# Performance work log

Hardware: AMD Instinct MI355X
Metric: run time of the kernel (lower is better)

Reference implementation:

```python
import jax, jax.numpy as jnp
import numpy as np

DIM = 1024          # n_embd
NUM_EXPERTS = 8
TOP_K = 2
HIDDEN = 4 * DIM // TOP_K   # expert_hidden_dim = 2048
BS, SLEN = 1, 2048


def setup_inputs() -> dict:
    key = jax.random.key(0)
    k0, k1, k2, k3 = jax.random.split(key, 4)
    x = jax.random.normal(k0, (BS, SLEN, DIM), dtype=jnp.float32)
    gate_w = jax.random.normal(k1, (NUM_EXPERTS, DIM), dtype=jnp.float32) * 0.02
    w_up = jax.random.normal(k2, (NUM_EXPERTS, HIDDEN, DIM), dtype=jnp.float32) * 0.02
    w_down = jax.random.normal(k3, (NUM_EXPERTS, DIM, HIDDEN), dtype=jnp.float32) * 0.02
    expert_bias = jnp.zeros((NUM_EXPERTS,), dtype=jnp.float32)
    return {"x": x, "gate_w": gate_w, "w_up": w_up, "w_down": w_down,
            "expert_bias": expert_bias}


def _moe(x, gate_w, w_up, w_down, expert_bias):
    bs, slen, dim = x.shape
    xf = x.reshape(-1, dim)                       # (T, D)
    # Sigmoid router (scores in fp32, bias only affects selection, not weights)
    scores = jax.nn.sigmoid(xf @ gate_w.T)        # (T, E)
    biased = scores + expert_bias
    _, sel = jax.lax.top_k(biased, TOP_K)         # (T, K) expert ids, distinct per token
    top_scores = jnp.take_along_axis(scores, sel, axis=-1)  # (T, K)

    # Scatter/gather dispatch + grouped GEMM is mathematically equivalent to:
    #   out[t] = sum_k W_down[e_tk] @ relu(W_up[e_tk] @ (s_tk * x[t]))^2
    # Loop over the small fixed expert set via lax.scan; unassigned tokens
    # contribute exactly zero (relu(0)^2 = 0), honoring the routing sparsity.
    def body(acc, ew):
        e, wu, wd = ew
        # combined routing weight for this expert per token (at most one slot)
        w_t = jnp.sum(jnp.where(sel == e, top_scores, 0.0), axis=-1)  # (T,)
        xe = xf * w_t[:, None]                    # (T, D), zero for non-routed
        h = jnp.square(jax.nn.relu(xe @ wu.T))    # (T, H)  relu(x)^2 activation
        return acc + h @ wd.T, None

    out0 = jnp.zeros_like(xf)
    out, _ = jax.lax.scan(body, out0, (jnp.arange(NUM_EXPERTS), w_up, w_down))
    return out.reshape(bs, slen, dim)


def reference(x, gate_w, w_up, w_down, expert_bias):
    return _moe(x, gate_w, w_up, w_down, expert_bias)
```

## Files before the change

kernel.cpp:

```cpp
#include <hip/hip_runtime.h>
#include <cstdint>
#include <cstddef>

#define T_TOK 2048
#define DMODEL 1024
#define NEXP 8
#define HID 2048
#define DUMP_ID 4096
#define NB_CONV 8192

typedef __bf16 bf16x8 __attribute__((ext_vector_type(8)));
typedef float f32x4 __attribute__((ext_vector_type(4)));
typedef unsigned short u16;
typedef u16 u16x8 __attribute__((ext_vector_type(8)));

__device__ __forceinline__ u16 f2bf(float f) {
    union { float f; unsigned int u; } v; v.f = f;
    unsigned int u = v.u;
    unsigned int r = (u + 0x7FFFu + ((u >> 16) & 1u)) >> 16;
    return (u16)r;
}

__device__ __forceinline__ void gl2lds16(const void* g, void* l) {
    __builtin_amdgcn_global_load_lds(
        (const __attribute__((address_space(1))) void*)g,
        (__attribute__((address_space(3))) void*)l,
        16, 0, 0);
}

__global__ __launch_bounds__(256) void fused_pre(
    const float4* __restrict__ wu4, const float4* __restrict__ wd4,
    ushort4* __restrict__ wub4, ushort4* __restrict__ wdb4,
    const float4* __restrict__ x4, const float4* __restrict__ gw4,
    const float* __restrict__ bias, ushort4* __restrict__ xb4,
    unsigned int* __restrict__ selpack, float* __restrict__ w2,
    unsigned int* __restrict__ xb_dump_row_u32) {
    const int b = blockIdx.x;
    const int tid = threadIdx.x;

    if (b < NB_CONV) {
        const int n4u = NEXP * HID * DMODEL / 4;
        int i0 = b * 256 + tid;
#pragma unroll
        for (int c = 0; c < 4; ++c) {
            int idx = i0 + c * (NB_CONV * 256);
            float4 f = (idx < n4u) ? wu4[idx] : wd4[idx - n4u];
            ushort4 o;
            o.x = f2bf(f.x); o.y = f2bf(f.y); o.z = f2bf(f.z); o.w = f2bf(f.w);
            if (idx < n4u) wub4[idx] = o; else wdb4[idx - n4u] = o;
        }
        return;
    }
    if (b == NB_CONV + 256) {
        if (tid < DMODEL / 2) xb_dump_row_u32[tid] = 0;
        return;
    }
    const int rb = b - NB_CONV;
    const int wv = tid >> 6;
    const int lane = tid & 63;
    const int pair = rb * 4 + wv;
    const int t0 = 2 * pair, t1 = t0 + 1;

    float acc0[NEXP], acc1[NEXP];
#pragma unroll
    for (int e = 0; e < NEXP; ++e) { acc0[e] = 0.f; acc1[e] = 0.f; }
#pragma unroll
    for (int j = 0; j < 4; ++j) {
        int i4 = lane + j * 64;
        float4 a0 = x4[t0 * 256 + i4];
        float4 a1 = x4[t1 * 256 + i4];
        ushort4 s0, s1;
        s0.x = f2bf(a0.x); s0.y = f2bf(a0.y); s0.z = f2bf(a0.z); s0.w = f2bf(a0.w);
        s1.x = f2bf(a1.x); s1.y = f2bf(a1.y); s1.z = f2bf(a1.z); s1.w = f2bf(a1.w);
        xb4[t0 * 256 + i4] = s0;
        xb4[t1 * 256 + i4] = s1;
#pragma unroll
        for (int e = 0; e < NEXP; ++e) {
            float4 g = gw4[e * 256 + i4];
            acc0[e] += a0.x * g.x + a0.y * g.y + a0.z * g.z + a0.w * g.w;
            acc1[e] += a1.x * g.x + a1.y * g.y + a1.z * g.z + a1.w * g.w;
        }
    }
#pragma unroll
    for (int e = 0; e < NEXP; ++e)
        for (int off = 32; off > 0; off >>= 1) {
            acc0[e] += __shfl_xor(acc0[e], off, 64);
            acc1[e] += __shfl_xor(acc1[e], off, 64);
        }
    if (lane == 0) {
#pragma unroll
        for (int tt = 0; tt < 2; ++tt) {
            int t = tt ? t1 : t0;
            float sc[NEXP], bi[NEXP];
#pragma unroll
            for (int e = 0; e < NEXP; ++e) {
                float a = tt ? acc1[e] : acc0[e];
                sc[e] = 1.f / (1.f + expf(-a));
                bi[e] = sc[e] + bias[e];
            }
            int e0 = 0;
            for (int e = 1; e < NEXP; ++e) if (bi[e] > bi[e0]) e0 = e;
            int e1 = -1;
            for (int e = 0; e < NEXP; ++e) {
                if (e == e0) continue;
                if (e1 < 0 || bi[e] > bi[e1]) e1 = e;
            }
            selpack[t] = (unsigned int)e0 | ((unsigned int)e1 << 8);
            w2[2 * t]     = sc[e0] * sc[e0];
            w2[2 * t + 1] = sc[e1] * sc[e1];
        }
    }
}

__global__ __launch_bounds__(256) void build_lists(
    const unsigned int* __restrict__ selpack, int* __restrict__ counts,
    int* __restrict__ list) {
    const int e = blockIdx.x;
    const int tid = threadIdx.x;
    const int lane = tid & 63;
    const int wv = tid >> 6;
    __shared__ int wsum[4];
    __shared__ int base;
    if (tid == 0) base = 0;
    __syncthreads();
    for (int tb = 0; tb < T_TOK; tb += 256) {
        int t = tb + tid;
        unsigned int sp = selpack[t];
        bool f1 = ((sp >> 8) & 255u) == (unsigned)e;
        bool f = ((sp & 255u) == (unsigned)e) | f1;
        int id = 2 * t + (f1 ? 1 : 0);
        unsigned long long m = __ballot(f);
        int pos = __popcll(m & ((1ull << lane) - 1ull));
        if (lane == 0) wsum[wv] = __popcll(m);
        __syncthreads();
        int woff = 0;
#pragma unroll
        for (int i = 0; i < 4; ++i) if (i < wv) woff += wsum[i];
        int bse = base;
        if (f) list[e * T_TOK + bse + woff + pos] = id;
        __syncthreads();
        if (tid == 0) base = bse + wsum[0] + wsum[1] + wsum[2] + wsum[3];
    }
    __syncthreads();
    int total = base;
    if (tid == 0) counts[e] = total;
    for (int i = total + tid; i < T_TOK; i += 256) list[e * T_TOK + i] = DUMP_ID;
}

template <int MODE>
__global__ __launch_bounds__(256, 2) void moe_gemm(
    const u16* __restrict__ Asrc, const int* __restrict__ list,
    const int* __restrict__ counts, const u16* __restrict__ Ball,
    const float* __restrict__ w2, u16* __restrict__ Hout,
    float* __restrict__ Cout) {
    constexpr int K   = (MODE == 0) ? DMODEL : HID;
    constexpr int N   = (MODE == 0) ? HID : DMODEL;
    constexpr int NKT = K / 64;
    constexpr int NTN = N / 128;
    constexpr int LOGNTN = (MODE == 0) ? 4 : 3;

    const int b = blockIdx.x;
    const int e = b & 7;
    const int rest = b >> 3;
    const int m0 = (rest >> LOGNTN) * 128;
    if (m0 >= counts[e]) return;
    const int n0 = (rest & (NTN - 1)) * 128;

    const int tid = threadIdx.x;
    const int lane = tid & 63;
    const int w = tid >> 6;

    __shared__ u16 As[128 * 64];
    __shared__ u16 Bs[128 * 64];

    const int* mylist = list + e * T_TOK + m0;
    const u16* B = Ball + (size_t)e * HID * DMODEL;

    const u16* ap[4];
    const u16* bp[4];
#pragma unroll
    for (int it = 0; it < 4; ++it) {
        int row = it * 32 + (tid >> 3);
        int gs = (tid & 7) ^ (row & 7);
        int id = mylist[row];
        int arow = (MODE == 0) ? (id >> 1) : id;
        ap[it] = Asrc + (size_t)arow * K + gs * 8;
        bp[it] = B + (size_t)(n0 + row) * K + gs * 8;
    }

    const int wm = (w >> 1) * 64;
    const int wn = (w & 1) * 64;
    const int quad = lane >> 4;
    const int lrow = lane & 15;

    f32x4 acc[4][4];
#pragma unroll
    for (int i = 0; i < 4; ++i)
#pragma unroll
        for (int j = 0; j < 4; ++j) acc[i][j] = f32x4{0.f, 0.f, 0.f, 0.f};

    for (int kt = 0; kt < NKT; ++kt) {
#pragma unroll
        for (int it = 0; it < 4; ++it)
            gl2lds16(ap[it] + kt * 64, &As[(it * 256 + w * 64) * 8]);
#pragma unroll
        for (int it = 0; it < 4; ++it)
            gl2lds16(bp[it] + kt * 64, &Bs[(it * 256 + w * 64) * 8]);
        __syncthreads();
#pragma unroll
        for (int s = 0; s < 2; ++s) {
            const int q = s * 4 + quad;
            bf16x8 af[4], bfr[4];
#pragma unroll
            for (int i = 0; i < 4; ++i) {
                int ra = wm + i * 16 + lrow;
                int rb = wn + i * 16 + lrow;
                af[i]  = *(const bf16x8*)&As[ra * 64 + (q ^ (ra & 7)) * 8];
                bfr[i] = *(const bf16x8*)&Bs[rb * 64 + (q ^ (rb & 7)) * 8];
            }
#pragma unroll
            for (int i = 0; i < 4; ++i)
#pragma unroll
                for (int j = 0; j < 4; ++j)
                    acc[i][j] = __builtin_amdgcn_mfma_f32_16x16x32_bf16(
                        af[i], bfr[j], acc[i][j], 0, 0, 0);
        }
        __syncthreads();
    }

#pragma unroll
    for (int i = 0; i < 4; ++i) {
        int mbase = wm + i * 16 + (lane >> 4) * 4;
        int ids[4];
        float ww[4];
#pragma unroll
        for (int r = 0; r < 4; ++r) {
            ids[r] = mylist[mbase + r];
            if (MODE == 0) ww[r] = w2[ids[r]];
        }
#pragma unroll
        for (int j = 0; j < 4; ++j) {
            int n = n0 + wn + j * 16 + (lane & 15);
#pragma unroll
            for (int r = 0; r < 4; ++r) {
                float v = acc[i][j][r];
                if (MODE == 0) {
                    v = (v > 0.f) ? v * v * ww[r] : 0.f;
                    Hout[(size_t)ids[r] * HID + n] = f2bf(v);
                } else {
                    if (ids[r] != DUMP_ID)
                        atomicAdd(&Cout[(size_t)(ids[r] >> 1) * DMODEL + n], v);
                }
            }
        }
    }
}

extern "C" void kernel_launch(void* const* d_in, const int* in_sizes, int n_in,
                              void* d_out, int out_size, void* d_ws, size_t ws_size,
                              hipStream_t stream) {
    const float* x      = (const float*)d_in[0];
    const float* gate_w = (const float*)d_in[1];
    const float* w_up   = (const float*)d_in[2];
    const float* w_down = (const float*)d_in[3];
    const float* bias   = (const float*)d_in[4];
    float* out = (float*)d_out;

    char* p = (char*)d_ws;
    int* counts = (int*)p;                 p += 256;
    int* list   = (int*)p;                 p += NEXP * T_TOK * 4;
    float* w2   = (float*)p;               p += 4104 * 4;
    unsigned int* selpack = (unsigned int*)p;  p += T_TOK * 4;
    u16* xb  = (u16*)p;  p += (size_t)(T_TOK + 1) * DMODEL * 2;
    u16* wub = (u16*)p;  p += (size_t)NEXP * HID * DMODEL * 2;
    u16* wdb = (u16*)p;  p += (size_t)NEXP * HID * DMODEL * 2;
    u16* h   = (u16*)p;  p += (size_t)(2 * T_TOK + 1) * HID * 2;

    hipMemsetAsync(d_out, 0, (size_t)out_size * sizeof(float), stream);

    fused_pre<<<NB_CONV + 256 + 1, 256, 0, stream>>>(
        (const float4*)w_up, (const float4*)w_down,
        (ushort4*)wub, (ushort4*)wdb,
        (const float4*)x, (const float4*)gate_w, bias,
        (ushort4*)xb, selpack, w2,
        (unsigned int*)(xb + (size_t)T_TOK * DMODEL));

    build_lists<<<NEXP, 256, 0, stream>>>(selpack, counts, list);

    moe_gemm<0><<<16 * (HID / 128) * NEXP, 256, 0, stream>>>(
        xb, list, counts, wub, w2, h, nullptr);

    moe_gemm<1><<<16 * (DMODEL / 128) * NEXP, 256, 0, stream>>>(
        h, list, counts, wdb, w2, nullptr, out);
}
```

Measured before the change: 265.6 us.

## Overlap w_down bf16 conversion with the up-projection GEMM launch

The fp32-to-bf16 conversion of w_down moves out of the pre-processing kernel and into extra blocks appended to the first grouped GEMM. Those blocks can then overlap with the up-projection GEMM tiles, shortening the critical path of the pre-kernel. The trade-off is that conversion blocks compete with GEMM blocks for CUs and bandwidth, and block scheduling order decides how much overlap actually happens.

```diff
diff --git a/kernel.cpp b/kernel.cpp
--- a/kernel.cpp
+++ b/kernel.cpp
@@ -7,7 +7,7 @@
 #define NEXP 8
 #define HID 2048
 #define DUMP_ID 4096
-#define NB_CONV 8192
+#define NB_CONV 4096
 
 typedef __bf16 bf16x8 __attribute__((ext_vector_type(8)));
 typedef float f32x4 __attribute__((ext_vector_type(4)));
@@ -28,9 +28,22 @@
         16, 0, 0);
 }
 
+__device__ __forceinline__ void cvt_blk(const float4* __restrict__ src,
+                                        ushort4* __restrict__ dst,
+                                        int bc, int tid) {
+    const int S = NB_CONV * 256;
+    const int i0 = bc * 256 + tid;
+#pragma unroll
+    for (int c = 0; c < 4; ++c) {
+        float4 f = src[i0 + c * S];
+        ushort4 o;
+        o.x = f2bf(f.x); o.y = f2bf(f.y); o.z = f2bf(f.z); o.w = f2bf(f.w);
+        dst[i0 + c * S] = o;
+    }
+}
+
 __global__ __launch_bounds__(256) void fused_pre(
-    const float4* __restrict__ wu4, const float4* __restrict__ wd4,
-    ushort4* __restrict__ wub4, ushort4* __restrict__ wdb4,
+    const float4* __restrict__ wu4, ushort4* __restrict__ wub4,
     const float4* __restrict__ x4, const float4* __restrict__ gw4,
     const float* __restrict__ bias, ushort4* __restrict__ xb4,
     unsigned int* __restrict__ selpack, float* __restrict__ w2,
@@ -39,16 +52,7 @@
     const int tid = threadIdx.x;
 
     if (b < NB_CONV) {
-        const int n4u = NEXP * HID * DMODEL / 4;
-        int i0 = b * 256 + tid;
-#pragma unroll
-        for (int c = 0; c < 4; ++c) {
-            int idx = i0 + c * (NB_CONV * 256);
-            float4 f = (idx < n4u) ? wu4[idx] : wd4[idx - n4u];
-            ushort4 o;
-            o.x = f2bf(f.x); o.y = f2bf(f.y); o.z = f2bf(f.z); o.w = f2bf(f.w);
-            if (idx < n4u) wub4[idx] = o; else wdb4[idx - n4u] = o;
-        }
+        cvt_blk(wu4, wub4, b, tid);
         return;
     }
     if (b == NB_CONV + 256) {
@@ -152,21 +156,29 @@
     const u16* __restrict__ Asrc, const int* __restrict__ list,
     const int* __restrict__ counts, const u16* __restrict__ Ball,
     const float* __restrict__ w2, u16* __restrict__ Hout,
-    float* __restrict__ Cout) {
+    float* __restrict__ Cout,
+    const float4* __restrict__ cvt_src, ushort4* __restrict__ cvt_dst) {
     constexpr int K   = (MODE == 0) ? DMODEL : HID;
     constexpr int N   = (MODE == 0) ? HID : DMODEL;
     constexpr int NKT = K / 64;
     constexpr int NTN = N / 128;
     constexpr int LOGNTN = (MODE == 0) ? 4 : 3;
+    constexpr int GEMMB = (T_TOK / 128) * NTN * NEXP;
 
     const int b = blockIdx.x;
+    const int tid = threadIdx.x;
+
+    if (MODE == 0 && b >= GEMMB) {
+        cvt_blk(cvt_src, cvt_dst, b - GEMMB, tid);
+        return;
+    }
+
     const int e = b & 7;
     const int rest = b >> 3;
     const int m0 = (rest >> LOGNTN) * 128;
     if (m0 >= counts[e]) return;
     const int n0 = (rest & (NTN - 1)) * 128;
 
-    const int tid = threadIdx.x;
     const int lane = tid & 63;
     const int w = tid >> 6;
 
@@ -279,17 +291,18 @@
     hipMemsetAsync(d_out, 0, (size_t)out_size * sizeof(float), stream);
 
     fused_pre<<<NB_CONV + 256 + 1, 256, 0, stream>>>(
-        (const float4*)w_up, (const float4*)w_down,
-        (ushort4*)wub, (ushort4*)wdb,
+        (const float4*)w_up, (ushort4*)wub,
         (const float4*)x, (const float4*)gate_w, bias,
         (ushort4*)xb, selpack, w2,
         (unsigned int*)(xb + (size_t)T_TOK * DMODEL));
 
     build_lists<<<NEXP, 256, 0, stream>>>(selpack, counts, list);
 
-    moe_gemm<0><<<16 * (HID / 128) * NEXP, 256, 0, stream>>>(
-        xb, list, counts, wub, w2, h, nullptr);
+    moe_gemm<0><<<16 * (HID / 128) * NEXP + NB_CONV, 256, 0, stream>>>(
+        xb, list, counts, wub, w2, h, nullptr,
+        (const float4*)w_down, (ushort4*)wdb);
 
     moe_gemm<1><<<16 * (DMODEL / 128) * NEXP, 256, 0, stream>>>(
-        h, list, counts, wdb, w2, nullptr, out);
-}
+        h, list, counts, wdb, w2, nullptr, out,
+        nullptr, nullptr);
+}
```

Measured after the change: 274.3 us. 1.03x slower.

## Fuse fp32-to-bf16 weight conversion into grouped GEMM B-tile loads

Applied to the files above, without the earlier changes.

Removes the separate pre-pass that converted all expert up/down weights from fp32 to bf16 in a workspace. The GEMM kernels now read fp32 weights directly through registers, convert them to bf16 and write swizzled tiles into LDS, replacing the async global-to-LDS copy for B. This avoids writing and re-reading 64 MB of bf16 weights, but each weight tile is now read as fp32 (twice the bytes) by every M-tile that uses it. It also loses the direct-to-LDS load path and adds conversion ALU work inside the K loop.

```diff
diff --git a/kernel.cpp b/kernel.cpp
--- a/kernel.cpp
+++ b/kernel.cpp
@@ -7,7 +7,6 @@
 #define NEXP 8
 #define HID 2048
 #define DUMP_ID 4096
-#define NB_CONV 8192
 
 typedef __bf16 bf16x8 __attribute__((ext_vector_type(8)));
 typedef float f32x4 __attribute__((ext_vector_type(4)));
@@ -29,8 +28,6 @@
 }
 
 __global__ __launch_bounds__(256) void fused_pre(
-    const float4* __restrict__ wu4, const float4* __restrict__ wd4,
-    ushort4* __restrict__ wub4, ushort4* __restrict__ wdb4,
     const float4* __restrict__ x4, const float4* __restrict__ gw4,
     const float* __restrict__ bias, ushort4* __restrict__ xb4,
     unsigned int* __restrict__ selpack, float* __restrict__ w2,
@@ -38,27 +35,13 @@
     const int b = blockIdx.x;
     const int tid = threadIdx.x;
 
-    if (b < NB_CONV) {
-        const int n4u = NEXP * HID * DMODEL / 4;
-        int i0 = b * 256 + tid;
-#pragma unroll
-        for (int c = 0; c < 4; ++c) {
-            int idx = i0 + c * (NB_CONV * 256);
-            float4 f = (idx < n4u) ? wu4[idx] : wd4[idx - n4u];
-            ushort4 o;
-            o.x = f2bf(f.x); o.y = f2bf(f.y); o.z = f2bf(f.z); o.w = f2bf(f.w);
-            if (idx < n4u) wub4[idx] = o; else wdb4[idx - n4u] = o;
-        }
-        return;
-    }
-    if (b == NB_CONV + 256) {
+    if (b == 256) {
         if (tid < DMODEL / 2) xb_dump_row_u32[tid] = 0;
         return;
     }
-    const int rb = b - NB_CONV;
     const int wv = tid >> 6;
     const int lane = tid & 63;
-    const int pair = rb * 4 + wv;
+    const int pair = b * 4 + wv;
     const int t0 = 2 * pair, t1 = t0 + 1;
 
     float acc0[NEXP], acc1[NEXP];
@@ -150,7 +133,7 @@
 template <int MODE>
 __global__ __launch_bounds__(256, 2) void moe_gemm(
     const u16* __restrict__ Asrc, const int* __restrict__ list,
-    const int* __restrict__ counts, const u16* __restrict__ Ball,
+    const int* __restrict__ counts, const float* __restrict__ Ball32,
     const float* __restrict__ w2, u16* __restrict__ Hout,
     float* __restrict__ Cout) {
     constexpr int K   = (MODE == 0) ? DMODEL : HID;
@@ -174,18 +157,21 @@
     __shared__ u16 Bs[128 * 64];
 
     const int* mylist = list + e * T_TOK + m0;
-    const u16* B = Ball + (size_t)e * HID * DMODEL;
+    const float* B32 = Ball32 + (size_t)e * HID * DMODEL;
 
     const u16* ap[4];
-    const u16* bp[4];
+    const float4* bp[4];
+    int bwr[4];
+    const int c8 = tid & 7;
 #pragma unroll
     for (int it = 0; it < 4; ++it) {
         int row = it * 32 + (tid >> 3);
-        int gs = (tid & 7) ^ (row & 7);
+        int gs = c8 ^ (row & 7);
         int id = mylist[row];
         int arow = (MODE == 0) ? (id >> 1) : id;
         ap[it] = Asrc + (size_t)arow * K + gs * 8;
-        bp[it] = B + (size_t)(n0 + row) * K + gs * 8;
+        bp[it] = (const float4*)(B32 + (size_t)(n0 + row) * K) + c8 * 2;
+        bwr[it] = row * 64 + gs * 8;
     }
 
     const int wm = (w >> 1) * 64;
@@ -203,9 +189,21 @@
 #pragma unroll
         for (int it = 0; it < 4; ++it)
             gl2lds16(ap[it] + kt * 64, &As[(it * 256 + w * 64) * 8]);
-#pragma unroll
-        for (int it = 0; it < 4; ++it)
-            gl2lds16(bp[it] + kt * 64, &Bs[(it * 256 + w * 64) * 8]);
+        float4 bu[4][2];
+#pragma unroll
+        for (int it = 0; it < 4; ++it) {
+            bu[it][0] = bp[it][kt * 16];
+            bu[it][1] = bp[it][kt * 16 + 1];
+        }
+#pragma unroll
+        for (int it = 0; it < 4; ++it) {
+            u16x8 o;
+            o[0] = f2bf(bu[it][0].x); o[1] = f2bf(bu[it][0].y);
+            o[2] = f2bf(bu[it][0].z); o[3] = f2bf(bu[it][0].w);
+            o[4] = f2bf(bu[it][1].x); o[5] = f2bf(bu[it][1].y);
+            o[6] = f2bf(bu[it][1].z); o[7] = f2bf(bu[it][1].w);
+            *(u16x8*)&Bs[bwr[it]] = o;
+        }
         __syncthreads();
 #pragma unroll
         for (int s = 0; s < 2; ++s) {
@@ -272,15 +270,11 @@
     float* w2   = (float*)p;               p += 4104 * 4;
     unsigned int* selpack = (unsigned int*)p;  p += T_TOK * 4;
     u16* xb  = (u16*)p;  p += (size_t)(T_TOK + 1) * DMODEL * 2;
-    u16* wub = (u16*)p;  p += (size_t)NEXP * HID * DMODEL * 2;
-    u16* wdb = (u16*)p;  p += (size_t)NEXP * HID * DMODEL * 2;
     u16* h   = (u16*)p;  p += (size_t)(2 * T_TOK + 1) * HID * 2;
 
     hipMemsetAsync(d_out, 0, (size_t)out_size * sizeof(float), stream);
 
-    fused_pre<<<NB_CONV + 256 + 1, 256, 0, stream>>>(
-        (const float4*)w_up, (const float4*)w_down,
-        (ushort4*)wub, (ushort4*)wdb,
+    fused_pre<<<257, 256, 0, stream>>>(
         (const float4*)x, (const float4*)gate_w, bias,
         (ushort4*)xb, selpack, w2,
         (unsigned int*)(xb + (size_t)T_TOK * DMODEL));
@@ -288,8 +282,8 @@
     build_lists<<<NEXP, 256, 0, stream>>>(selpack, counts, list);
 
     moe_gemm<0><<<16 * (HID / 128) * NEXP, 256, 0, stream>>>(
-        xb, list, counts, wub, w2, h, nullptr);
+        xb, list, counts, w_up, w2, h, nullptr);
 
     moe_gemm<1><<<16 * (DMODEL / 128) * NEXP, 256, 0, stream>>>(
-        h, list, counts, wdb, w2, nullptr, out);
-}
+        h, list, counts, w_down, w2, nullptr, out);
+}
```

New measurement: 258.6 us. 2.6% less time.
